# Performance work log

Measured on AMD Instinct MI355X. Metric: run time of the kernel, lower is better.

## Reference

```python
import jax, jax.numpy as jnp
import numpy as np

DIM = 1024
H = 16
HKV = 4
HD = DIM // H  # 64
GROUP = H // HKV
ROPE_BASE = 10000.0
B, T = 2, 2048


def rms_norm(x, eps):
    return x * jax.lax.rsqrt(jnp.mean(x * x, axis=-1, keepdims=True) + eps)


def apply_rotary(x, cos, sin):
    # x: [B, h, T, HD]; cos/sin: [1, 1, T, HD//2]
    half = x.shape[-1] // 2
    x1, x2 = x[..., :half], x[..., half:]
    return jnp.concatenate([x1 * cos + x2 * sin, -x1 * sin + x2 * cos], axis=-1)


def setup_inputs() -> dict:
    key = jax.random.key(0)
    ks = jax.random.split(key, 5)
    s = 0.02
    return {
        "x": jax.random.normal(ks[0], (B, T, DIM), dtype=jnp.float32),
        "Wq": jax.random.normal(ks[1], (DIM, DIM), dtype=jnp.float32) * s,
        "Wk": jax.random.normal(ks[2], (HKV * HD, DIM), dtype=jnp.float32) * s,
        "Wv": jax.random.normal(ks[3], (HKV * HD, DIM), dtype=jnp.float32) * s,
        "Wproj": jax.random.normal(ks[4], (DIM, DIM), dtype=jnp.float32) * s,
        "q_gain": jnp.full((H,), 12.0, dtype=jnp.float32),
    }


def reference(x, Wq, Wk, Wv, Wproj, q_gain):
    bsz, seqlen, dim = x.shape
    eps = jnp.asarray(jnp.finfo(x.dtype).eps, x.dtype)

    # double RMSNorm path: normalized input for q/k, raw input for v
    x_qk = rms_norm(x, eps)
    q = (x_qk @ Wq.T).reshape(bsz, seqlen, H, HD).transpose(0, 2, 1, 3)    # [B,H,T,D]
    k = (x_qk @ Wk.T).reshape(bsz, seqlen, HKV, HD).transpose(0, 2, 1, 3)  # [B,Hkv,T,D]
    v = (x @ Wv.T).reshape(bsz, seqlen, HKV, HD).transpose(0, 2, 1, 3)     # [B,Hkv,T,D]

    q = rms_norm(q, eps)
    k = rms_norm(k, eps)

    # rotary embeddings
    t = jnp.arange(seqlen, dtype=jnp.float32)
    inv_freq = 1.0 / (ROPE_BASE ** (jnp.arange(0, HD, 2, dtype=jnp.float32) / HD))
    freqs = jnp.outer(t, inv_freq)                       # [T, HD//2]
    cos = jnp.cos(freqs)[None, None].astype(x.dtype)
    sin = jnp.sin(freqs)[None, None].astype(x.dtype)
    q = apply_rotary(q, cos, sin)
    k = apply_rotary(k, cos, sin)

    # per-head gain on q
    q = q * q_gain.astype(q.dtype)[None, :, None, None]

    # GQA: expand kv heads to query heads
    k_r = jnp.repeat(k, GROUP, axis=1)  # [B,H,T,D]
    v_r = jnp.repeat(v, GROUP, axis=1)

    scale = 1.0 / np.sqrt(HD)
    scores = jnp.einsum("bhqd,bhkd->bhqk", q, k_r) * scale
    causal = jnp.tril(jnp.ones((seqlen, seqlen), dtype=bool))
    scores = jnp.where(causal[None, None], scores, jnp.asarray(-jnp.inf, scores.dtype))
    attn = jax.nn.softmax(scores, axis=-1)
    y = jnp.einsum("bhqk,bhkd->bhqd", attn, v_r)          # [B,H,T,D]

    # XSA: remove value-direction component from output
    y_bt = y.transpose(0, 2, 1, 3)                        # [B,T,H,D]
    v_bt = v.transpose(0, 2, 1, 3)                        # [B,T,Hkv,D]
    y_g = y_bt.reshape(bsz, seqlen, HKV, GROUP, HD)
    vnorm = jnp.sqrt(jnp.sum(v_bt * v_bt, axis=-1, keepdims=True))
    vn = (v_bt / jnp.maximum(vnorm, 1e-12))[..., None, :]  # [B,T,Hkv,1,D]
    proj = jnp.sum(y_g * vn, axis=-1, keepdims=True) * vn
    y_bt = (y_g - proj).reshape(bsz, seqlen, H, HD)

    return y_bt.reshape(bsz, seqlen, dim) @ Wproj.T
```

## Files before the change

kernel.cpp:

```cpp
#include <hip/hip_runtime.h>
#include <hip/hip_bf16.h>

typedef __attribute__((ext_vector_type(8))) short bf8v;
typedef __attribute__((ext_vector_type(4))) float f4v;

#define MFMA16(a,b,c) __builtin_amdgcn_mfma_f32_16x16x32_bf16((a),(b),(c),0,0,0)

#define GLD16(gp, lp) __builtin_amdgcn_global_load_lds( \
    (const __attribute__((address_space(1))) void*)(gp), \
    (__attribute__((address_space(3))) void*)(lp), 16, 0, 0)

#define DIMC   1024
#define TSEQ   2048
#define NH     16
#define NKV    4
#define HDIM   64
#define RMS_EPS 1.1920929e-07f
#define QSCALE 0.1803368801111601f

__device__ __forceinline__ ushort f2bf(float f) {
  unsigned u = __builtin_bit_cast(unsigned, f);
  u = (u + 0x7FFFu + ((u >> 16) & 1u)) >> 16;
  return (ushort)u;
}
__device__ __forceinline__ float bf2f(ushort u) {
  return __builtin_bit_cast(float, (unsigned)u << 16);
}
__device__ __forceinline__ unsigned cvtpk(float lo, float hi) {
  unsigned r;
  asm("v_cvt_pk_bf16_f32 %0, %1, %2" : "=v"(r) : "v"(lo), "v"(hi));
  return r;
}

__global__ __launch_bounds__(256) void prep_all(
    const float* __restrict__ x,
    const float* __restrict__ Wq, const float* __restrict__ Wk,
    const float* __restrict__ Wv, const float* __restrict__ Wp,
    ushort* __restrict__ xhi, ushort* __restrict__ xlo,
    ushort* __restrict__ xb,
    ushort* __restrict__ wqkh, ushort* __restrict__ wqkl,
    ushort* __restrict__ wvb, ushort* __restrict__ wpb,
    float* __restrict__ cosT, float* __restrict__ sinT) {
  __shared__ float red[4];
  int bid = blockIdx.x, tid = threadIdx.x;
  if (bid < 4096) {
    int row = bid;
    int lane = tid & 63, w = tid >> 6;
    float4 v = ((const float4*)(x + (size_t)row * DIMC))[tid];
    float ss = v.x * v.x + v.y * v.y + v.z * v.z + v.w * v.w;
    for (int off = 32; off; off >>= 1) ss += __shfl_xor(ss, off);
    if (lane == 0) red[w] = ss;
    __syncthreads();
    float tot = red[0] + red[1] + red[2] + red[3];
    float rs = rsqrtf(tot * (1.0f / DIMC) + RMS_EPS);
    float n0 = v.x * rs, n1 = v.y * rs, n2 = v.z * rs, n3 = v.w * rs;
    ushort4 h, l, ob;
    h.x = f2bf(n0); l.x = f2bf(n0 - bf2f(h.x));
    h.y = f2bf(n1); l.y = f2bf(n1 - bf2f(h.y));
    h.z = f2bf(n2); l.z = f2bf(n2 - bf2f(h.z));
    h.w = f2bf(n3); l.w = f2bf(n3 - bf2f(h.w));
    ob.x = f2bf(v.x); ob.y = f2bf(v.y); ob.z = f2bf(v.z); ob.w = f2bf(v.w);
    ((ushort4*)(xhi + (size_t)row * DIMC))[tid] = h;
    ((ushort4*)(xlo + (size_t)row * DIMC))[tid] = l;
    ((ushort4*)(xb  + (size_t)row * DIMC))[tid] = ob;
    return;
  }
  int wb = bid - 4096;
  if (wb < 1280) {
    const float* src;
    size_t si, di;
    if (wb < 1024) { src = Wq; si = (size_t)wb * 256 + tid; di = si; }
    else { src = Wk; si = (size_t)(wb - 1024) * 256 + tid; di = 262144 + si; }
    float4 v = ((const float4*)src)[si];
    ushort4 h, l;
    h.x = f2bf(v.x); l.x = f2bf(v.x - bf2f(h.x));
    h.y = f2bf(v.y); l.y = f2bf(v.y - bf2f(h.y));
    h.z = f2bf(v.z); l.z = f2bf(v.z - bf2f(h.z));
    h.w = f2bf(v.w); l.w = f2bf(v.w - bf2f(h.w));
    ((ushort4*)wqkh)[di] = h;
    ((ushort4*)wqkl)[di] = l;
  } else if (wb < 2560) {
    const float* src;
    ushort* dst;
    int i;
    if (wb < 1536) { src = Wv; dst = wvb; i = (wb - 1280) * 256 + tid; }
    else           { src = Wp; dst = wpb; i = (wb - 1536) * 256 + tid; }
    float4 v = ((const float4*)src)[i];
    ushort4 o;
    o.x = f2bf(v.x); o.y = f2bf(v.y); o.z = f2bf(v.z); o.w = f2bf(v.w);
    ((ushort4*)dst)[i] = o;
  } else {
    int i = (wb - 2560) * 256 + tid;
    int t = i >> 5, j = i & 31;
    float inv = 1.0f / powf(10000.0f, (float)j * (1.0f / 32.0f));
    float f = (float)t * inv;
    cosT[i] = cosf(f);
    sinT[i] = sinf(f);
  }
}

__global__ __launch_bounds__(256, 2)
void gemm_qkv(const ushort* __restrict__ xhi, const ushort* __restrict__ xlo,
              const ushort* __restrict__ wqkh, const ushort* __restrict__ wqkl,
              float* __restrict__ QKf, const ushort* __restrict__ xb,
              const ushort* __restrict__ wvb, float* __restrict__ Vf) {
  __shared__ __align__(16) ushort lA[128 * 64];
  __shared__ __align__(16) ushort lB[128 * 64];
  const int bx = blockIdx.x;
  const bool vpath = (bx >= 10);
  const ushort* A0 = vpath ? xb : xhi;
  const ushort* A1 = vpath ? xb : xlo;
  const ushort* B0 = vpath ? wvb : wqkh;
  const ushort* B1 = vpath ? wvb : wqkl;
  float* C = vpath ? Vf : QKf;
  const int N = vpath ? 256 : 1280;
  const int n0 = vpath ? (bx - 10) * 128 : bx * 128;
  const int nseg = vpath ? 1 : 3;

  const int t = threadIdx.x;
  const int lane = t & 63, w = t >> 6;
  const int wr = w >> 1, wc = w & 1;
  const int l15 = lane & 15, lg = lane >> 4;
  const int m0 = blockIdx.y * 128;
  const int srow = t >> 3, scp = t & 7;

  f4v acc[4][4] = {};

  for (int k0 = 0; k0 < nseg * 1024; k0 += 64) {
    const int seg = k0 >> 10, kk = k0 & 1023;
    const ushort* Ab = (seg == 1) ? A1 : A0;
    const ushort* Bb = (seg == 2) ? B1 : B0;
    for (int i = 0; i < 4; ++i) {
      int row = srow + i * 32;
      int sc = scp ^ (row & 7);
      const ushort* ga = Ab + (size_t)(m0 + row) * DIMC + kk + sc * 8;
      const ushort* gb = Bb + (size_t)(n0 + row) * DIMC + kk + sc * 8;
      GLD16(ga, &lA[w * 512 + i * 2048]);
      GLD16(gb, &lB[w * 512 + i * 2048]);
    }
    __syncthreads();
    for (int kx = 0; kx < 2; ++kx) {
      bf8v af[4], bfr[4];
      for (int m = 0; m < 4; ++m) {
        int row = wr * 64 + m * 16 + l15;
        int ch = (kx * 4 + lg) ^ (row & 7);
        af[m] = *(const bf8v*)&lA[row * 64 + ch * 8];
      }
      for (int n = 0; n < 4; ++n) {
        int row = wc * 64 + n * 16 + l15;
        int ch = (kx * 4 + lg) ^ (row & 7);
        bfr[n] = *(const bf8v*)&lB[row * 64 + ch * 8];
      }
      for (int m = 0; m < 4; ++m)
        for (int n = 0; n < 4; ++n)
          acc[m][n] = MFMA16(af[m], bfr[n], acc[m][n]);
    }
    __syncthreads();
  }

  for (int m = 0; m < 4; ++m)
    for (int n = 0; n < 4; ++n)
      for (int j = 0; j < 4; ++j) {
        int r = m0 + wr * 64 + m * 16 + lg * 4 + j;
        int c = n0 + wc * 64 + n * 16 + l15;
        C[(size_t)r * N + c] = acc[m][n][j];
      }
}

__global__ __launch_bounds__(256, 2)
void gemm_bt(const ushort* __restrict__ A0, const ushort* __restrict__ B0,
             float* __restrict__ C, int N) {
  __shared__ __align__(16) ushort lA[128 * 64];
  __shared__ __align__(16) ushort lB[128 * 64];
  const int t = threadIdx.x;
  const int lane = t & 63, w = t >> 6;
  const int wr = w >> 1, wc = w & 1;
  const int l15 = lane & 15, lg = lane >> 4;
  const int m0 = blockIdx.y * 128, n0 = blockIdx.x * 128;
  const int srow = t >> 3, scp = t & 7;

  f4v acc[4][4] = {};

  for (int k0 = 0; k0 < 1024; k0 += 64) {
    for (int i = 0; i < 4; ++i) {
      int row = srow + i * 32;
      int sc = scp ^ (row & 7);
      const ushort* ga = A0 + (size_t)(m0 + row) * DIMC + k0 + sc * 8;
      const ushort* gb = B0 + (size_t)(n0 + row) * DIMC + k0 + sc * 8;
      GLD16(ga, &lA[w * 512 + i * 2048]);
      GLD16(gb, &lB[w * 512 + i * 2048]);
    }
    __syncthreads();
    for (int kx = 0; kx < 2; ++kx) {
      bf8v af[4], bfr[4];
      for (int m = 0; m < 4; ++m) {
        int row = wr * 64 + m * 16 + l15;
        int ch = (kx * 4 + lg) ^ (row & 7);
        af[m] = *(const bf8v*)&lA[row * 64 + ch * 8];
      }
      for (int n = 0; n < 4; ++n) {
        int row = wc * 64 + n * 16 + l15;
        int ch = (kx * 4 + lg) ^ (row & 7);
        bfr[n] = *(const bf8v*)&lB[row * 64 + ch * 8];
      }
      for (int m = 0; m < 4; ++m)
        for (int n = 0; n < 4; ++n)
          acc[m][n] = MFMA16(af[m], bfr[n], acc[m][n]);
    }
    __syncthreads();
  }

  for (int m = 0; m < 4; ++m)
    for (int n = 0; n < 4; ++n)
      for (int j = 0; j < 4; ++j) {
        int r = m0 + wr * 64 + m * 16 + lg * 4 + j;
        int c = n0 + wc * 64 + n * 16 + l15;
        C[(size_t)r * N + c] = acc[m][n][j];
      }
}

__global__ __launch_bounds__(256) void post_all(
    const float* __restrict__ QKf, const float* __restrict__ cosT,
    const float* __restrict__ sinT, const float* __restrict__ qgain,
    ushort* __restrict__ qhi, ushort* __restrict__ qlo,
    ushort* __restrict__ kb16,
    const float* __restrict__ Vf, ushort* __restrict__ vt2,
    ushort* __restrict__ vhat_t) {
  __shared__ float lds[64][69];
  __shared__ float rnv[64];
  int bid = blockIdx.x;
  if (bid < 4096) {
    int m = bid;
    int b = m >> 11, tpos = m & 2047;
    int lane = threadIdx.x & 63, w = threadIdx.x >> 6;
    int d = lane, j = d & 31;
    float sgn = (d < 32) ? 1.0f : -1.0f;
    float c = cosT[tpos * 32 + j], s = sinT[tpos * 32 + j];

    for (int i = 0; i < 4; ++i) {
      int h = w * 4 + i;
      float q = QKf[(size_t)m * 1280 + h * HDIM + d];
      float ss = q * q;
      for (int off = 32; off; off >>= 1) ss += __shfl_xor(ss, off);
      float rs = rsqrtf(ss * (1.0f / HDIM) + RMS_EPS);
      float qn = q * rs;
      float partner = __shfl_xor(qn, 32);
      float ro = (qn * c + sgn * partner * s) * (qgain[h] * QSCALE);
      ushort hi = f2bf(ro);
      ushort lo = f2bf(ro - bf2f(hi));
      size_t idx = (((size_t)b * NH + h) * TSEQ + tpos) * HDIM + d;
      qhi[idx] = hi;
      qlo[idx] = lo;
    }
    {
      int kv = w;
      float k = QKf[(size_t)m * 1280 + 1024 + kv * HDIM + d];
      float ss = k * k;
      for (int off = 32; off; off >>= 1) ss += __shfl_xor(ss, off);
      float rs = rsqrtf(ss * (1.0f / HDIM) + RMS_EPS);
      float kn = k * rs;
      float partner = __shfl_xor(kn, 32);
      float ro = kn * c + sgn * partner * s;
      kb16[((size_t)(b * NKV + kv) * TSEQ + tpos) * HDIM + d] = f2bf(ro);
    }
    return;
  }
  {
    int vb = bid - 4096;
    int bkv = vb >> 5, tt = vb & 31;
    int b = bkv >> 2, kv = bkv & 3;
    int tid = threadIdx.x;
    for (int i = 0; i < 16; ++i) {
      int idx = i * 256 + tid;
      int tloc = idx >> 6, d = idx & 63;
      lds[d][tloc] = Vf[((size_t)(b * TSEQ + tt * 64 + tloc)) * 256 + kv * 64 + d];
    }
    __syncthreads();
    {
      int t = tid >> 2, prt = tid & 3;
      float ssum = 0.f;
      for (int dd = 0; dd < 16; ++dd) {
        float v = lds[prt * 16 + dd][t];
        ssum += v * v;
      }
      ssum += __shfl_xor(ssum, 1);
      ssum += __shfl_xor(ssum, 2);
      if (prt == 0) rnv[t] = 1.0f / fmaxf(sqrtf(ssum), 1e-12f);
    }
    __syncthreads();
    for (int i = 0; i < 16; ++i) {
      int idx = i * 256 + tid;
      int d = idx >> 6, tloc = idx & 63;
      float v = lds[d][tloc];
      vt2[(size_t)bkv * (TSEQ * 64) + tt * 4096 + d * 64 + tloc] = f2bf(v);
      vhat_t[(size_t)bkv * (TSEQ * 64) + (size_t)d * TSEQ + tt * 64 + tloc] = f2bf(v * rnv[tloc]);
    }
  }
}

__global__ __launch_bounds__(256, 4) void attn_kern(
    const ushort* __restrict__ qhi, const ushort* __restrict__ qlo,
    const ushort* __restrict__ kb16, const ushort* __restrict__ vt2,
    const ushort* __restrict__ vhat_t, ushort* __restrict__ ytil) {
  __shared__ __align__(16) ushort lk[2][64 * 64];
  __shared__ __align__(16) ushort lv[2][64 * 64];
  __shared__ __align__(16) unsigned pl[4][512];
  const int t = threadIdx.x;
  const int lane = t & 63, w = t >> 6;
  const int bid = blockIdx.x;
  const int xcd = bid & 7, g = (bid >> 3) & 3, trank = bid >> 5;
  const int ta = trank & 7, tq = trank >> 3;
  const int tile = (tq == 0) ? (31 - ta)
                 : (tq == 1) ? ta
                 : (tq == 2) ? (23 - ta)
                             : (8 + ta);
  const int b = xcd >> 2, kv = xcd & 3, h = kv * 4 + g;
  const int l15 = lane & 15, lg = lane >> 4;
  const int q0 = tile * 64 + w * 16;
  const int ntile = tile + 1;
  const int t3 = t >> 3, tc8 = t & 7;
  const int rx = l15 & 7;
  const int pswz = rx << 2;

  const size_t qoff = (((size_t)(b * NH + h)) * TSEQ + q0 + l15) * HDIM;
  bf8v bq0h = *(const bf8v*)(qhi + qoff + lg * 8);
  bf8v bq1h = *(const bf8v*)(qhi + qoff + 32 + lg * 8);
  bf8v bq0l = *(const bf8v*)(qlo + qoff + lg * 8);
  bf8v bq1l = *(const bf8v*)(qlo + qoff + 32 + lg * 8);

  const ushort* kb = kb16 + (size_t)(b * NKV + kv) * TSEQ * 64;
  const ushort* vb = vt2 + (size_t)(b * NKV + kv) * TSEQ * 64;
  unsigned* pw = &pl[w][0];

#define STAGE(BUF, IT) do { \
    _Pragma("unroll") \
    for (int i = 0; i < 2; ++i) { \
      int row = i * 32 + t3; \
      int sc = tc8 ^ (row & 7); \
      GLD16(kb + (size_t)((IT) * 64 + row) * 64 + sc * 8, \
            &lk[BUF][(i * 32 + (w << 3)) * 64]); \
      GLD16(vb + (size_t)(IT) * 4096 + row * 64 + sc * 8, \
            &lv[BUF][(i * 32 + (w << 3)) * 64]); \
    } } while (0)

  STAGE(0, 0);

  f4v y[4] = {};
  float mrow = -1e30f, lrow = 0.f;

#pragma unroll 1
  for (int it = 0; it < ntile; ++it) {
    const int cur = it & 1;
    __syncthreads();
    if (it + 1 < ntile) STAGE(cur ^ 1, it + 1);

    const ushort* lkc = &lk[cur][0];
    const ushort* lvc = &lv[cur][0];
    const int kv0 = it * 64;

    f4v s[4];
    __builtin_amdgcn_s_setprio(1);
#pragma unroll
    for (int n = 0; n < 4; ++n) {
      const ushort* krow = lkc + (n * 16 + l15) * 64;
      bf8v kh0 = *(const bf8v*)&krow[((0 + lg) ^ rx) * 8];
      bf8v kh1 = *(const bf8v*)&krow[((4 + lg) ^ rx) * 8];
      f4v z = {};
      f4v acc = MFMA16(kh0, bq0h, z);
      acc = MFMA16(kh1, bq1h, acc);
      acc = MFMA16(kh0, bq0l, acc);
      acc = MFMA16(kh1, bq1l, acc);
      s[n] = acc;
    }
    __builtin_amdgcn_s_setprio(0);

    const bool need_mask = (it == ntile - 1);
    float mloc = -1e30f;
#pragma unroll
    for (int n = 0; n < 4; ++n)
#pragma unroll
      for (int j = 0; j < 4; ++j) {
        float v = s[n][j];
        if (need_mask && (kv0 + n * 16 + lg * 4 + j > q0 + l15)) v = -1e30f;
        s[n][j] = v;
        mloc = fmaxf(mloc, v);
      }
    mloc = fmaxf(mloc, __shfl_xor(mloc, 16));
    mloc = fmaxf(mloc, __shfl_xor(mloc, 32));
    if (__any(mloc > mrow + 11.5f)) {
      float mnew = fmaxf(mrow, mloc);
      float scf = exp2f(mrow - mnew);
      lrow *= scf;
#pragma unroll
      for (int n = 0; n < 4; ++n) y[n] *= scf;
      mrow = mnew;
    }
    float rs = 0.f;
#pragma unroll
    for (int n = 0; n < 4; ++n)
#pragma unroll
      for (int j = 0; j < 4; ++j) {
        float e = exp2f(s[n][j] - mrow);
        s[n][j] = e;
        rs += e;
      }
    rs += __shfl_xor(rs, 16);
    rs += __shfl_xor(rs, 32);
    lrow += rs;

#pragma unroll
    for (int n = 0; n < 4; ++n) {
      uint2 pk;
      pk.x = cvtpk(s[n][0], s[n][1]);
      pk.y = cvtpk(s[n][2], s[n][3]);
      *(uint2*)&pw[l15 * 32 + ((8 * n + 2 * lg) ^ pswz)] = pk;
    }
    asm volatile("s_waitcnt lgkmcnt(0)" ::: "memory");
    bf8v pb0 = *(const bf8v*)&pw[l15 * 32 + ((lg * 4) ^ pswz)];
    bf8v pb1 = *(const bf8v*)&pw[l15 * 32 + ((16 + lg * 4) ^ pswz)];
    __builtin_amdgcn_s_setprio(1);
#pragma unroll
    for (int n = 0; n < 4; ++n) {
      const ushort* vrow = lvc + (n * 16 + l15) * 64;
      bf8v va0 = *(const bf8v*)&vrow[((0 + lg) ^ rx) * 8];
      bf8v va1 = *(const bf8v*)&vrow[((4 + lg) ^ rx) * 8];
      y[n] = MFMA16(va0, pb0, y[n]);
      y[n] = MFMA16(va1, pb1, y[n]);
    }
    __builtin_amdgcn_s_setprio(0);
  }
#undef STAGE

  {
    float inv = 1.0f / lrow;
    const ushort* vh = vhat_t + (size_t)(b * NKV + kv) * TSEQ * 64;
    ushort* yw = (ushort*)pw;
    float vv[4][4];
    float dp = 0.f;
#pragma unroll
    for (int n = 0; n < 4; ++n)
#pragma unroll
      for (int j = 0; j < 4; ++j) {
        int d = n * 16 + lg * 4 + j;
        float yv = y[n][j] * inv;
        y[n][j] = yv;
        vv[n][j] = bf2f(vh[(size_t)d * TSEQ + q0 + l15]);
        dp += yv * vv[n][j];
      }
    dp += __shfl_xor(dp, 16);
    dp += __shfl_xor(dp, 32);
#pragma unroll
    for (int n = 0; n < 4; ++n)
#pragma unroll
      for (int j = 0; j < 4; ++j) {
        int d = n * 16 + lg * 4 + j;
        yw[l15 * 64 + (((d >> 3) ^ rx) << 3) + (d & 7)] = f2bf(y[n][j] - dp * vv[n][j]);
      }
    asm volatile("s_waitcnt lgkmcnt(0)" ::: "memory");
    int row = lane >> 2, quad = lane & 3;
    bf8v y0 = *(const bf8v*)(yw + row * 64 + ((quad ^ (row & 7)) << 3));
    bf8v y1 = *(const bf8v*)(yw + row * 64 + (((quad + 4) ^ (row & 7)) << 3));
    size_t gbase = ((size_t)(b * TSEQ + q0 + row)) * DIMC + h * HDIM + quad * 8;
    *(bf8v*)(ytil + gbase) = y0;
    *(bf8v*)(ytil + gbase + 32) = y1;
  }
}

extern "C" void kernel_launch(void* const* d_in, const int* in_sizes, int n_in,
                              void* d_out, int out_size, void* d_ws, size_t ws_size,
                              hipStream_t stream) {
  (void)in_sizes; (void)n_in; (void)out_size; (void)ws_size;
  const float* x  = (const float*)d_in[0];
  const float* Wq = (const float*)d_in[1];
  const float* Wk = (const float*)d_in[2];
  const float* Wv = (const float*)d_in[3];
  const float* Wp = (const float*)d_in[4];
  const float* qg = (const float*)d_in[5];
  float* out = (float*)d_out;
  char* ws = (char*)d_ws;
  const size_t KB = 1024, MB = 1ull << 20;

  ushort* xhi = (ushort*)(ws);
  ushort* xlo = (ushort*)(ws + 8 * MB);
  ushort* xb  = (ushort*)(ws + 16 * MB);
  ushort* wqkh = (ushort*)(ws + 24 * MB);
  ushort* wqkl = (ushort*)(ws + 26 * MB + 512 * KB);
  ushort* wvb = (ushort*)(ws + 29 * MB);
  ushort* wpb = (ushort*)(ws + 29 * MB + 512 * KB);
  float*  cosT = (float*)(ws + 31 * MB + 512 * KB);
  float*  sinT = (float*)(ws + 31 * MB + 768 * KB);
  float*  QKf  = (float*)(ws + 32 * MB);
  ushort* kb16 = (ushort*)(ws + 52 * MB);
  ushort* vt2  = (ushort*)(ws + 54 * MB);
  ushort* vhat = (ushort*)(ws + 56 * MB);

  float*  Vf   = out;
  ushort* qhb  = xhi;
  ushort* qlb  = xlo;
  ushort* ytil = xb;

  prep_all<<<6912, 256, 0, stream>>>(x, Wq, Wk, Wv, Wp, xhi, xlo, xb,
                                     wqkh, wqkl, wvb, wpb, cosT, sinT);

  gemm_qkv<<<dim3(12, 32), 256, 0, stream>>>(xhi, xlo, wqkh, wqkl, QKf,
                                             xb, wvb, Vf);

  post_all<<<4352, 256, 0, stream>>>(QKf, cosT, sinT, qg, qhb, qlb, kb16,
                                     Vf, vt2, vhat);
  attn_kern<<<1024, 256, 0, stream>>>(qhb, qlb, kb16, vt2, vhat, ytil);
  gemm_bt<<<dim3(8, 32), 256, 0, stream>>>(ytil, wpb, out, 1024);
}
```

Before: 153.7 us.

## Split-K the QK projection GEMM into hi and correction blocks for better load balance

The 3-segment QK GEMM (hi*hi + lo*hi + hi*lo) is split into two independent blocks. A 16-step block computes hi*hi into fp32, and a 32-step block computes the two cross terms and stores them as bf16 into spare output memory. post_all then sums the two parts, and the grid is flattened to 704 blocks interleaved by size, with launch bounds raised to 3 blocks per SM. This aims to spread the long 48-step tiles across more CUs. It costs an extra bf16 write and read, and the correction term is rounded to bf16.

```diff
diff --git a/kernel.cpp b/kernel.cpp
--- a/kernel.cpp
+++ b/kernel.cpp
@@ -99,37 +99,50 @@
   }
 }
 
-__global__ __launch_bounds__(256, 2)
+__global__ __launch_bounds__(256, 3)
 void gemm_qkv(const ushort* __restrict__ xhi, const ushort* __restrict__ xlo,
               const ushort* __restrict__ wqkh, const ushort* __restrict__ wqkl,
-              float* __restrict__ QKf, const ushort* __restrict__ xb,
-              const ushort* __restrict__ wvb, float* __restrict__ Vf) {
+              float* __restrict__ QKf, ushort* __restrict__ QKc,
+              const ushort* __restrict__ xb, const ushort* __restrict__ wvb,
+              float* __restrict__ Vf) {
   __shared__ __align__(16) ushort lA[128 * 64];
   __shared__ __align__(16) ushort lB[128 * 64];
-  const int bx = blockIdx.x;
-  const bool vpath = (bx >= 10);
-  const ushort* A0 = vpath ? xb : xhi;
-  const ushort* A1 = vpath ? xb : xlo;
-  const ushort* B0 = vpath ? wvb : wqkh;
-  const ushort* B1 = vpath ? wvb : wqkl;
-  float* C = vpath ? Vf : QKf;
-  const int N = vpath ? 256 : 1280;
-  const int n0 = vpath ? (bx - 10) * 128 : bx * 128;
-  const int nseg = vpath ? 1 : 3;
+  const int bid = blockIdx.x;
+  int u;
+  bool big;
+  if (bid < 256)      { big = true;  u = bid; }
+  else if (bid < 448) { big = false; u = bid - 256; }
+  else if (bid < 512) { big = true;  u = 256 + (bid - 448); }
+  else                { big = false; u = 192 + (bid - 512); }
+
+  const ushort *Ap0, *Bp0, *Ap1, *Bp1;
+  float* Cf = QKf;
+  int N = 1280, nsteps, mt, n0;
+  if (big) {
+    mt = u / 10; n0 = (u % 10) * 128;
+    Ap0 = xlo; Bp0 = wqkh; Ap1 = xhi; Bp1 = wqkl; nsteps = 32;
+  } else if (u < 320) {
+    mt = u / 10; n0 = (u % 10) * 128;
+    Ap0 = xhi; Bp0 = wqkh; Ap1 = Ap0; Bp1 = Bp0; nsteps = 16;
+  } else {
+    int v = u - 320; mt = v >> 1; n0 = (v & 1) * 128;
+    Ap0 = xb; Bp0 = wvb; Ap1 = Ap0; Bp1 = Bp0; nsteps = 16;
+    Cf = Vf; N = 256;
+  }
+  const int m0 = mt * 128;
 
   const int t = threadIdx.x;
   const int lane = t & 63, w = t >> 6;
   const int wr = w >> 1, wc = w & 1;
   const int l15 = lane & 15, lg = lane >> 4;
-  const int m0 = blockIdx.y * 128;
   const int srow = t >> 3, scp = t & 7;
 
   f4v acc[4][4] = {};
 
-  for (int k0 = 0; k0 < nseg * 1024; k0 += 64) {
-    const int seg = k0 >> 10, kk = k0 & 1023;
-    const ushort* Ab = (seg == 1) ? A1 : A0;
-    const ushort* Bb = (seg == 2) ? B1 : B0;
+  for (int s = 0; s < nsteps; ++s) {
+    const ushort* Ab = (s < 16) ? Ap0 : Ap1;
+    const ushort* Bb = (s < 16) ? Bp0 : Bp1;
+    const int kk = (s & 15) * 64;
     for (int i = 0; i < 4; ++i) {
       int row = srow + i * 32;
       int sc = scp ^ (row & 7);
@@ -158,13 +171,23 @@
     __syncthreads();
   }
 
-  for (int m = 0; m < 4; ++m)
-    for (int n = 0; n < 4; ++n)
-      for (int j = 0; j < 4; ++j) {
-        int r = m0 + wr * 64 + m * 16 + lg * 4 + j;
-        int c = n0 + wc * 64 + n * 16 + l15;
-        C[(size_t)r * N + c] = acc[m][n][j];
-      }
+  if (big) {
+    for (int m = 0; m < 4; ++m)
+      for (int n = 0; n < 4; ++n)
+        for (int j = 0; j < 4; ++j) {
+          int r = m0 + wr * 64 + m * 16 + lg * 4 + j;
+          int c = n0 + wc * 64 + n * 16 + l15;
+          QKc[(size_t)r * 1280 + c] = f2bf(acc[m][n][j]);
+        }
+  } else {
+    for (int m = 0; m < 4; ++m)
+      for (int n = 0; n < 4; ++n)
+        for (int j = 0; j < 4; ++j) {
+          int r = m0 + wr * 64 + m * 16 + lg * 4 + j;
+          int c = n0 + wc * 64 + n * 16 + l15;
+          Cf[(size_t)r * N + c] = acc[m][n][j];
+        }
+  }
 }
 
 __global__ __launch_bounds__(256, 2)
@@ -220,7 +243,8 @@
 }
 
 __global__ __launch_bounds__(256) void post_all(
-    const float* __restrict__ QKf, const float* __restrict__ cosT,
+    const float* __restrict__ QKf, const ushort* __restrict__ QKc,
+    const float* __restrict__ cosT,
     const float* __restrict__ sinT, const float* __restrict__ qgain,
     ushort* __restrict__ qhi, ushort* __restrict__ qlo,
     ushort* __restrict__ kb16,
@@ -239,7 +263,8 @@
 
     for (int i = 0; i < 4; ++i) {
       int h = w * 4 + i;
-      float q = QKf[(size_t)m * 1280 + h * HDIM + d];
+      size_t base = (size_t)m * 1280 + h * HDIM + d;
+      float q = QKf[base] + bf2f(QKc[base]);
       float ss = q * q;
       for (int off = 32; off; off >>= 1) ss += __shfl_xor(ss, off);
       float rs = rsqrtf(ss * (1.0f / HDIM) + RMS_EPS);
@@ -254,7 +279,8 @@
     }
     {
       int kv = w;
-      float k = QKf[(size_t)m * 1280 + 1024 + kv * HDIM + d];
+      size_t base = (size_t)m * 1280 + 1024 + kv * HDIM + d;
+      float k = QKf[base] + bf2f(QKc[base]);
       float ss = k * k;
       for (int off = 32; off; off >>= 1) ss += __shfl_xor(ss, off);
       float rs = rsqrtf(ss * (1.0f / HDIM) + RMS_EPS);
@@ -495,6 +521,7 @@
   ushort* vhat = (ushort*)(ws + 56 * MB);
 
   float*  Vf   = out;
+  ushort* QKc  = (ushort*)((char*)out + 4 * MB);
   ushort* qhb  = xhi;
   ushort* qlb  = xlo;
   ushort* ytil = xb;
@@ -502,10 +529,10 @@
   prep_all<<<6912, 256, 0, stream>>>(x, Wq, Wk, Wv, Wp, xhi, xlo, xb,
                                      wqkh, wqkl, wvb, wpb, cosT, sinT);
 
-  gemm_qkv<<<dim3(12, 32), 256, 0, stream>>>(xhi, xlo, wqkh, wqkl, QKf,
-                                             xb, wvb, Vf);
-
-  post_all<<<4352, 256, 0, stream>>>(QKf, cosT, sinT, qg, qhb, qlb, kb16,
+  gemm_qkv<<<704, 256, 0, stream>>>(xhi, xlo, wqkh, wqkl, QKf, QKc,
+                                    xb, wvb, Vf);
+
+  post_all<<<4352, 256, 0, stream>>>(QKf, QKc, cosT, sinT, qg, qhb, qlb, kb16,
                                      Vf, vt2, vhat);
   attn_kern<<<1024, 256, 0, stream>>>(qhb, qlb, kb16, vt2, vhat, ytil);
   gemm_bt<<<dim3(8, 32), 256, 0, stream>>>(ytil, wpb, out, 1024);
```

Result: faster. 143.6 us (-6.6%).
